# Kernel optimization log

Hardware: AMD Instinct MI355X
Metric: run time of the kernel (lower is better)

## Reference

```python
import jax, jax.numpy as jnp
import numpy as np

N_NODES = 150000
N_EDGES = 2400000
IN_DIM, HID, OUT_DIM = 2, 32, 1


def gcn_conv(x, edge_index, W, b, n_nodes):
    """PyG-style GCNConv: add self-loops, sym-normalize, aggregate, linear."""
    h = x @ W  # [N, F_out] linear first (as in PyG GCNConv)
    loop = jnp.arange(n_nodes)
    src = jnp.concatenate([edge_index[0], loop])
    dst = jnp.concatenate([edge_index[1], loop])
    deg = jax.ops.segment_sum(jnp.ones(src.shape[0], h.dtype), dst,
                              num_segments=n_nodes)  # in-degree incl. self-loops
    dinv = jnp.where(deg > 0, jax.lax.rsqrt(deg), 0.0)
    norm = dinv[src] * dinv[dst]  # [E+N]
    msg = h[src] * norm[:, None]  # gather + scale
    out = jax.ops.segment_sum(msg, dst, num_segments=n_nodes)  # scatter-add
    return out + b


def setup_inputs() -> dict:
    key = jax.random.key(0)
    ks = jax.random.split(key, 8)
    x = jax.random.normal(ks[0], (N_NODES, IN_DIM), dtype=jnp.float32)
    edge_index = jax.random.randint(ks[1], (2, N_EDGES), 0, N_NODES, dtype=jnp.int32)
    W1 = jax.random.normal(ks[2], (IN_DIM, HID), dtype=jnp.float32) / np.sqrt(IN_DIM)
    b1 = jnp.zeros((HID,), jnp.float32)
    W2 = jax.random.normal(ks[3], (HID, HID), dtype=jnp.float32) / np.sqrt(HID)
    b2 = jnp.zeros((HID,), jnp.float32)
    Wp = jax.random.normal(ks[4], (HID, OUT_DIM), dtype=jnp.float32) / np.sqrt(HID)
    bp = jnp.zeros((OUT_DIM,), jnp.float32)
    return {"x": x, "edge_index": edge_index, "W1": W1, "b1": b1,
            "W2": W2, "b2": b2, "Wp": Wp, "bp": bp}


def reference(x, edge_index, W1, b1, W2, b2, Wp, bp):
    n = x.shape[0]
    h = jax.nn.relu(gcn_conv(x, edge_index, W1, b1, n))
    h = jax.nn.relu(gcn_conv(h, edge_index, W2, b2, n))
    return jax.nn.sigmoid(h @ Wp + bp)  # [N, 1]
```

## Files before the change

### kernel.cpp

```cpp
#include <hip/hip_runtime.h>

#define HID 32
#define SH 9
#define BNODES 512
#define NBMAX 320
#define TILE 8192
#define CAP 16384
#define STAGECAP 12288

typedef unsigned int uint;

__device__ __forceinline__ uint f2bf(float v) {
    uint b = __float_as_uint(v);
    return (b + 0x7fffu + ((b >> 16) & 1u)) >> 16;
}

__global__ void k_zero(int* __restrict__ p, int n) {
    int i = blockIdx.x * 256 + threadIdx.x;
    if (i < n) p[i] = 0;
}

__global__ void __launch_bounds__(512) k_bucketize(
        const int* __restrict__ src, const int* __restrict__ dst,
        int* __restrict__ bcur, uint* __restrict__ ebuf, int E, int NB) {
    __shared__ uint  ecache[TILE];
    __shared__ unsigned short bcache[TILE];
    __shared__ int cnt[NBMAX];
    __shared__ int loff[NBMAX + 1];
    __shared__ int gbase[NBMAX];
    int tid = threadIdx.x;
    int tbase = blockIdx.x * TILE;
    int tcount = min(E - tbase, TILE);
    int tc4 = tcount >> 2;
    const int4* dst4 = (const int4*)(dst + tbase);
    const int4* src4 = (const int4*)(src + tbase);

    for (int b = tid; b < NBMAX; b += 512) cnt[b] = 0;
    __syncthreads();
#pragma unroll
    for (int k = 0; k < TILE / 4 / 512; ++k) {
        int q = k * 512 + tid;
        if (q < tc4) {
            int4 d = dst4[q];
            atomicAdd(&cnt[d.x >> SH], 1);
            atomicAdd(&cnt[d.y >> SH], 1);
            atomicAdd(&cnt[d.z >> SH], 1);
            atomicAdd(&cnt[d.w >> SH], 1);
        }
    }
    if (tid == 0)
        for (int t = tc4 << 2; t < tcount; ++t) atomicAdd(&cnt[dst[tbase + t] >> SH], 1);
    __syncthreads();
    if (tid < 64) {
        int lo = tid * 5;
        int s = 0;
        for (int b = lo; b < lo + 5 && b < NB; ++b) s += cnt[b];
        int v = s;
        for (int off = 1; off < 64; off <<= 1) {
            int u = __shfl_up(v, off, 64);
            if (tid >= off) v += u;
        }
        int excl = v - s;
        for (int b = lo; b < lo + 5 && b < NB; ++b) { loff[b] = excl; excl += cnt[b]; }
        if (tid == 63) loff[NB] = excl;
    }
    __syncthreads();
    for (int b = tid; b < NB; b += 512) cnt[b] = loff[b];
    __syncthreads();
#pragma unroll
    for (int k = 0; k < TILE / 4 / 512; ++k) {
        int q = k * 512 + tid;
        if (q < tc4) {
            int4 d = dst4[q];
            int4 s = src4[q];
            int b0 = d.x >> SH, p0 = atomicAdd(&cnt[b0], 1);
            ecache[p0] = (uint)s.x | ((uint)(d.x & (BNODES - 1)) << 18); bcache[p0] = (unsigned short)b0;
            int b1 = d.y >> SH, p1_ = atomicAdd(&cnt[b1], 1);
            ecache[p1_] = (uint)s.y | ((uint)(d.y & (BNODES - 1)) << 18); bcache[p1_] = (unsigned short)b1;
            int b2 = d.z >> SH, p2_ = atomicAdd(&cnt[b2], 1);
            ecache[p2_] = (uint)s.z | ((uint)(d.z & (BNODES - 1)) << 18); bcache[p2_] = (unsigned short)b2;
            int b3 = d.w >> SH, p3_ = atomicAdd(&cnt[b3], 1);
            ecache[p3_] = (uint)s.w | ((uint)(d.w & (BNODES - 1)) << 18); bcache[p3_] = (unsigned short)b3;
        }
    }
    if (tid == 0)
        for (int t = tc4 << 2; t < tcount; ++t) {
            int d = dst[tbase + t];
            int b_ = d >> SH;
            int pos = atomicAdd(&cnt[b_], 1);
            ecache[pos] = (uint)src[tbase + t] | ((uint)(d & (BNODES - 1)) << 18);
            bcache[pos] = (unsigned short)b_;
        }
    __syncthreads();
    for (int b = tid; b < NB; b += 512) {
        int tc = loff[b + 1] - loff[b];
        if (tc > 0) gbase[b] = b * CAP + atomicAdd(&bcur[b], tc);
    }
    __syncthreads();
    for (int j = tid; j < tcount; j += 512) {
        int b = bcache[j];
        ebuf[gbase[b] + (j - loff[b])] = ecache[j];
    }
}

__global__ void k_scanb(const int* __restrict__ bcur, int* __restrict__ bbase,
                        int* __restrict__ rowptr, int N, int NB) {
    __shared__ int l[NBMAX + 1];
    int tid = threadIdx.x;
    if (tid < 64) {
        int lo = tid * 5;
        int s = 0;
        for (int b = lo; b < lo + 5 && b < NB; ++b) s += bcur[b];
        int v = s;
        for (int off = 1; off < 64; off <<= 1) {
            int u = __shfl_up(v, off, 64);
            if (tid >= off) v += u;
        }
        int excl = v - s;
        for (int b = lo; b < lo + 5 && b < NB; ++b) { l[b] = excl; excl += bcur[b]; }
        if (tid == 63) l[NB] = excl;
    }
    __syncthreads();
    for (int b = tid; b <= NB; b += blockDim.x) bbase[b] = l[b];
    if (tid == 0) rowptr[N] = l[NB];
}

__global__ void __launch_bounds__(512) k_sortb(
        const uint* __restrict__ ebuf, const int* __restrict__ bcur,
        const int* __restrict__ bbase, const float* __restrict__ x,
        int* __restrict__ rowptr, float* __restrict__ dinv,
        float2* __restrict__ p1, int* __restrict__ col, int N) {
    __shared__ int c[BNODES];
    __shared__ int off[BNODES];
    __shared__ int cur[BNODES];
    __shared__ uint stage[STAGECAP];
    int b = blockIdx.x, tid = threadIdx.x;
    int cnt = bcur[b];
    const uint* eb = ebuf + (long)b * CAP;
    int cbase = bbase[b];
    for (int t = tid; t < BNODES; t += 512) c[t] = 0;
    __syncthreads();
    int vc = cnt >> 2;
    const uint4* e4 = (const uint4*)eb;
    for (int q = tid; q < vc; q += 512) {
        uint4 e = e4[q];
        atomicAdd(&c[e.x >> 18], 1);
        atomicAdd(&c[e.y >> 18], 1);
        atomicAdd(&c[e.z >> 18], 1);
        atomicAdd(&c[e.w >> 18], 1);
        int j = q << 2;
        if (j + 3 < STAGECAP) {
            stage[j] = e.x; stage[j + 1] = e.y; stage[j + 2] = e.z; stage[j + 3] = e.w;
        }
    }
    for (int j = (vc << 2) + tid; j < cnt; j += 512) {
        uint e = eb[j];
        atomicAdd(&c[e >> 18], 1);
        if (j < STAGECAP) stage[j] = e;
    }
    __syncthreads();
    if (tid < 64) {
        int lo = tid * 8, s = 0;
#pragma unroll
        for (int k = 0; k < 8; ++k) s += c[lo + k];
        int v = s;
        for (int o = 1; o < 64; o <<= 1) {
            int u = __shfl_up(v, o, 64);
            if (tid >= o) v += u;
        }
        int excl = v - s;
#pragma unroll
        for (int k = 0; k < 8; ++k) { off[lo + k] = excl; excl += c[lo + k]; }
    }
    __syncthreads();
    for (int t = tid; t < BNODES; t += 512) {
        cur[t] = off[t];
        int node = (b << SH) + t;
        if (node < N) {
            rowptr[node] = cbase + off[t];
            float di = rsqrtf((float)c[t] + 1.0f);
            dinv[node] = di;
            float2 xv = ((const float2*)x)[node];
            p1[node] = make_float2(xv.x * di, xv.y * di);
        }
    }
    __syncthreads();
    int lim = min(cnt, STAGECAP);
    for (int j = tid; j < lim; j += 512) {
        uint e = stage[j];
        int dl = e >> 18;
        int pos = atomicAdd(&cur[dl], 1);
        col[cbase + pos] = (int)(e & 0x3FFFF);
    }
    for (int j = STAGECAP + tid; j < cnt; j += 512) {
        uint e = eb[j];
        int dl = e >> 18;
        int pos = atomicAdd(&cur[dl], 1);
        col[cbase + pos] = (int)(e & 0x3FFFF);
    }
}

__global__ void __launch_bounds__(256) k_gl12(
        const int* __restrict__ rowptr, const int* __restrict__ col,
        const float2* __restrict__ p1, const float* __restrict__ dinv,
        const float* __restrict__ W1, const float* __restrict__ b1,
        const float* __restrict__ W2, uint* __restrict__ p2h, int N) {
    __shared__ float sW1[64], sb1[32], sW2[HID * HID];
    int tid = threadIdx.x;
    for (int t = tid; t < HID * HID; t += 256) sW2[t] = W2[t];
    if (tid < 64) sW1[tid] = W1[tid];
    if (tid < 32) sb1[tid] = b1[tid];
    __syncthreads();
    int i = blockIdx.x * 16 + (tid >> 4);
    if (i >= N) return;
    int sub = tid & 15;

    int beg = rowptr[i], end = rowptr[i + 1];
    float ax = 0, ay = 0, bx = 0, by = 0;
    int j = beg + sub;
    for (; j + 16 < end; j += 32) {
        int c0 = col[j], c1 = col[j + 16];
        float2 v0 = p1[c0], v1 = p1[c1];
        ax += v0.x; ay += v0.y;
        bx += v1.x; by += v1.y;
    }
    if (j < end) {
        float2 v = p1[col[j]];
        ax += v.x; ay += v.y;
    }
    float sx = ax + bx, sy = ay + by;
#pragma unroll
    for (int m = 1; m < 16; m <<= 1) {
        sx += __shfl_xor(sx, m, 16);
        sy += __shfl_xor(sy, m, 16);
    }

    float2 a = p1[i];
    float di = dinv[i];
    float g0 = di * (a.x + sx);
    float g1 = di * (a.y + sy);

    float h0 = fmaxf(g0 * sW1[2 * sub] + g1 * sW1[32 + 2 * sub] + sb1[2 * sub], 0.0f);
    float h1 = fmaxf(g0 * sW1[2 * sub + 1] + g1 * sW1[32 + 2 * sub + 1] + sb1[2 * sub + 1], 0.0f);

    float o0 = 0, o1 = 0;
    int fb = 2 * sub;
#pragma unroll
    for (int s = 0; s < 16; ++s) {
        float hk0 = __shfl(h0, s, 16);
        float hk1 = __shfl(h1, s, 16);
        const float* w0 = &sW2[(2 * s) * HID + fb];
        const float* w1 = &sW2[(2 * s + 1) * HID + fb];
        o0 += hk0 * w0[0]; o1 += hk0 * w0[1];
        o0 += hk1 * w1[0]; o1 += hk1 * w1[1];
    }

    p2h[(long)i * 16 + sub] = f2bf(di * o0) | (f2bf(di * o1) << 16);
}

__global__ void k_gout(const int* __restrict__ rowptr, const int* __restrict__ col,
                       const uint* __restrict__ p2h, const float* __restrict__ b2,
                       const float* __restrict__ Wp, const float* __restrict__ bp,
                       const float* __restrict__ dinv, float* __restrict__ out, int N) {
    int node = blockIdx.x * 16 + (threadIdx.x >> 4);
    if (node >= N) return;
    int hl = threadIdx.x & 15;
    int beg = rowptr[node], end = rowptr[node + 1];
    uint w = p2h[(long)node * 16 + hl];
    float sA0 = __uint_as_float(w << 16), sB0 = __uint_as_float(w & 0xffff0000u);
    float sA1 = 0, sB1 = 0, sA2 = 0, sB2 = 0, sA3 = 0, sB3 = 0;
    float sA4 = 0, sB4 = 0, sA5 = 0, sB5 = 0, sA6 = 0, sB6 = 0, sA7 = 0, sB7 = 0;
    int j = beg;
    for (; j + 8 <= end; j += 8) {
        int c0 = col[j],     c1 = col[j + 1], c2 = col[j + 2], c3 = col[j + 3];
        int c4 = col[j + 4], c5 = col[j + 5], c6 = col[j + 6], c7 = col[j + 7];
        uint w0 = p2h[(long)c0 * 16 + hl];
        uint w1 = p2h[(long)c1 * 16 + hl];
        uint w2 = p2h[(long)c2 * 16 + hl];
        uint w3 = p2h[(long)c3 * 16 + hl];
        uint w4 = p2h[(long)c4 * 16 + hl];
        uint w5 = p2h[(long)c5 * 16 + hl];
        uint w6 = p2h[(long)c6 * 16 + hl];
        uint w7 = p2h[(long)c7 * 16 + hl];
        sA0 += __uint_as_float(w0 << 16); sB0 += __uint_as_float(w0 & 0xffff0000u);
        sA1 += __uint_as_float(w1 << 16); sB1 += __uint_as_float(w1 & 0xffff0000u);
        sA2 += __uint_as_float(w2 << 16); sB2 += __uint_as_float(w2 & 0xffff0000u);
        sA3 += __uint_as_float(w3 << 16); sB3 += __uint_as_float(w3 & 0xffff0000u);
        sA4 += __uint_as_float(w4 << 16); sB4 += __uint_as_float(w4 & 0xffff0000u);
        sA5 += __uint_as_float(w5 << 16); sB5 += __uint_as_float(w5 & 0xffff0000u);
        sA6 += __uint_as_float(w6 << 16); sB6 += __uint_as_float(w6 & 0xffff0000u);
        sA7 += __uint_as_float(w7 << 16); sB7 += __uint_as_float(w7 & 0xffff0000u);
    }
    for (; j + 4 <= end; j += 4) {
        int c0 = col[j], c1 = col[j + 1], c2 = col[j + 2], c3 = col[j + 3];
        uint w0 = p2h[(long)c0 * 16 + hl];
        uint w1 = p2h[(long)c1 * 16 + hl];
        uint w2 = p2h[(long)c2 * 16 + hl];
        uint w3 = p2h[(long)c3 * 16 + hl];
        sA0 += __uint_as_float(w0 << 16); sB0 += __uint_as_float(w0 & 0xffff0000u);
        sA1 += __uint_as_float(w1 << 16); sB1 += __uint_as_float(w1 & 0xffff0000u);
        sA2 += __uint_as_float(w2 << 16); sB2 += __uint_as_float(w2 & 0xffff0000u);
        sA3 += __uint_as_float(w3 << 16); sB3 += __uint_as_float(w3 & 0xffff0000u);
    }
    for (; j < end; ++j) {
        uint wj = p2h[(long)col[j] * 16 + hl];
        sA0 += __uint_as_float(wj << 16); sB0 += __uint_as_float(wj & 0xffff0000u);
    }
    float sA = ((sA0 + sA1) + (sA2 + sA3)) + ((sA4 + sA5) + (sA6 + sA7));
    float sB = ((sB0 + sB1) + (sB2 + sB3)) + ((sB4 + sB5) + (sB6 + sB7));
    float di = dinv[node];
    float hvA = fmaxf(di * sA + b2[2 * hl], 0.0f);
    float hvB = fmaxf(di * sB + b2[2 * hl + 1], 0.0f);
    float v = hvA * Wp[2 * hl] + hvB * Wp[2 * hl + 1];
#pragma unroll
    for (int m = 8; m > 0; m >>= 1) v += __shfl_xor(v, m, 16);
    if (hl == 0) out[node] = 1.0f / (1.0f + expf(-(v + bp[0])));
}

extern "C" void kernel_launch(void* const* d_in, const int* in_sizes, int n_in,
                              void* d_out, int out_size, void* d_ws, size_t ws_size,
                              hipStream_t stream) {
    const float* x  = (const float*)d_in[0];
    const int*   ei = (const int*)d_in[1];
    const float* W1 = (const float*)d_in[2];
    const float* b1 = (const float*)d_in[3];
    const float* W2 = (const float*)d_in[4];
    const float* b2 = (const float*)d_in[5];
    const float* Wp = (const float*)d_in[6];
    const float* bp = (const float*)d_in[7];
    float* out = (float*)d_out;

    const int N = in_sizes[0] / 2;
    const int E = in_sizes[1] / 2;
    const int* src = ei;
    const int* dst = ei + E;
    const int NB = (N + BNODES - 1) >> SH;

    char* ws = (char*)d_ws;
    size_t off = 0;
    auto alloc = [&](size_t bytes) {
        void* ptr = ws + off;
        off += (bytes + 255) & ~(size_t)255;
        return ptr;
    };
    int*    bcur   = (int*)alloc((size_t)NBMAX * 4);
    int*    bbase  = (int*)alloc((size_t)(NBMAX + 1) * 4);
    int*    rowptr = (int*)alloc((size_t)(N + 1) * 4);
    float*  dinv   = (float*)alloc((size_t)N * 4);
    uint*   ebuf   = (uint*)alloc((size_t)NBMAX * CAP * 4);
    int*    col    = (int*)alloc((size_t)E * 4);
    float2* p1     = (float2*)alloc((size_t)N * 8);
    uint*   p2h    = (uint*)alloc((size_t)N * 16 * 4);

    const int nb_t = (E + TILE - 1) / TILE;
    const int nb_g = (N + 15) / 16;

    k_zero<<<(NBMAX + 255) / 256, 256, 0, stream>>>(bcur, NBMAX);
    k_bucketize<<<nb_t, 512, 0, stream>>>(src, dst, bcur, ebuf, E, NB);
    k_scanb<<<1, 256, 0, stream>>>(bcur, bbase, rowptr, N, NB);
    k_sortb<<<NB, 512, 0, stream>>>(ebuf, bcur, bbase, x, rowptr, dinv, p1, col, N);
    k_gl12<<<nb_g, 256, 0, stream>>>(rowptr, col, p1, dinv, W1, b1, W2, p2h, N);
    k_gout<<<nb_g, 256, 0, stream>>>(rowptr, col, p2h, b2, Wp, bp, dinv, out, N);
}
```

Measured before the change: 117.8 us.

## Sort nodes by degree within each bucket to balance aggregation work

In the bucket sort kernel, nodes in each 512-node bucket are counting-sorted by in-degree (capped at 63) into a node permutation. Both aggregation kernels then process nodes in that order, so the 16 nodes in a block and the 4 nodes in a wavefront have similar edge counts and less lane divergence and tail imbalance. The cost is an extra shared-memory histogram and scan in the sort kernel and one more indirection load per node group. Memory locality for rowptr and the output writes also becomes less regular.

```diff
diff --git a/kernel.cpp b/kernel.cpp
--- a/kernel.cpp
+++ b/kernel.cpp
@@ -129,16 +129,21 @@
         const uint* __restrict__ ebuf, const int* __restrict__ bcur,
         const int* __restrict__ bbase, const float* __restrict__ x,
         int* __restrict__ rowptr, float* __restrict__ dinv,
-        float2* __restrict__ p1, int* __restrict__ col, int N) {
+        float2* __restrict__ p1, int* __restrict__ col,
+        int* __restrict__ nodeperm, int N) {
     __shared__ int c[BNODES];
     __shared__ int off[BNODES];
     __shared__ int cur[BNODES];
+    __shared__ int dbin[64];
+    __shared__ int dcur[64];
     __shared__ uint stage[STAGECAP];
     int b = blockIdx.x, tid = threadIdx.x;
     int cnt = bcur[b];
     const uint* eb = ebuf + (long)b * CAP;
     int cbase = bbase[b];
+    int nnodes = min(BNODES, N - (b << SH));
     for (int t = tid; t < BNODES; t += 512) c[t] = 0;
+    if (tid < 64) dbin[tid] = 0;
     __syncthreads();
     int vc = cnt >> 2;
     const uint4* e4 = (const uint4*)eb;
@@ -183,6 +188,26 @@
             float2 xv = ((const float2*)x)[node];
             p1[node] = make_float2(xv.x * di, xv.y * di);
         }
+        if (t < nnodes) atomicAdd(&dbin[min(c[t], 63)], 1);
+    }
+    __syncthreads();
+    if (tid < 64) {
+        int orig = dbin[tid];
+        int v = orig;
+        for (int o = 1; o < 64; o <<= 1) {
+            int u = __shfl_up(v, o, 64);
+            if (tid >= o) v += u;
+        }
+        dcur[tid] = v - orig;
+    }
+    __syncthreads();
+    for (int t = tid; t < BNODES; t += 512) {
+        if (t < nnodes) {
+            int r = atomicAdd(&dcur[min(c[t], 63)], 1);
+            nodeperm[(b << SH) + r] = (b << SH) + t;
+        } else {
+            nodeperm[(b << SH) + t] = N;
+        }
     }
     __syncthreads();
     int lim = min(cnt, STAGECAP);
@@ -201,17 +226,20 @@
 }
 
 __global__ void __launch_bounds__(256) k_gl12(
+        const int* __restrict__ nodeperm,
         const int* __restrict__ rowptr, const int* __restrict__ col,
         const float2* __restrict__ p1, const float* __restrict__ dinv,
         const float* __restrict__ W1, const float* __restrict__ b1,
-        const float* __restrict__ W2, uint* __restrict__ p2h, int N) {
+        const float* __restrict__ W2, uint* __restrict__ p2h, int N, int NTOT) {
     __shared__ float sW1[64], sb1[32], sW2[HID * HID];
     int tid = threadIdx.x;
     for (int t = tid; t < HID * HID; t += 256) sW2[t] = W2[t];
     if (tid < 64) sW1[tid] = W1[tid];
     if (tid < 32) sb1[tid] = b1[tid];
     __syncthreads();
-    int i = blockIdx.x * 16 + (tid >> 4);
+    int idx = blockIdx.x * 16 + (tid >> 4);
+    if (idx >= NTOT) return;
+    int i = nodeperm[idx];
     if (i >= N) return;
     int sub = tid & 15;
 
@@ -258,11 +286,15 @@
     p2h[(long)i * 16 + sub] = f2bf(di * o0) | (f2bf(di * o1) << 16);
 }
 
-__global__ void k_gout(const int* __restrict__ rowptr, const int* __restrict__ col,
+__global__ void k_gout(const int* __restrict__ nodeperm,
+                       const int* __restrict__ rowptr, const int* __restrict__ col,
                        const uint* __restrict__ p2h, const float* __restrict__ b2,
                        const float* __restrict__ Wp, const float* __restrict__ bp,
-                       const float* __restrict__ dinv, float* __restrict__ out, int N) {
-    int node = blockIdx.x * 16 + (threadIdx.x >> 4);
+                       const float* __restrict__ dinv, float* __restrict__ out,
+                       int N, int NTOT) {
+    int idx = blockIdx.x * 16 + (threadIdx.x >> 4);
+    if (idx >= NTOT) return;
+    int node = nodeperm[idx];
     if (node >= N) return;
     int hl = threadIdx.x & 15;
     int beg = rowptr[node], end = rowptr[node + 1];
@@ -335,6 +367,7 @@
     const int* src = ei;
     const int* dst = ei + E;
     const int NB = (N + BNODES - 1) >> SH;
+    const int NTOT = NB << SH;
 
     char* ws = (char*)d_ws;
     size_t off = 0;
@@ -343,22 +376,23 @@
         off += (bytes + 255) & ~(size_t)255;
         return ptr;
     };
-    int*    bcur   = (int*)alloc((size_t)NBMAX * 4);
-    int*    bbase  = (int*)alloc((size_t)(NBMAX + 1) * 4);
-    int*    rowptr = (int*)alloc((size_t)(N + 1) * 4);
-    float*  dinv   = (float*)alloc((size_t)N * 4);
-    uint*   ebuf   = (uint*)alloc((size_t)NBMAX * CAP * 4);
-    int*    col    = (int*)alloc((size_t)E * 4);
-    float2* p1     = (float2*)alloc((size_t)N * 8);
-    uint*   p2h    = (uint*)alloc((size_t)N * 16 * 4);
+    int*    bcur     = (int*)alloc((size_t)NBMAX * 4);
+    int*    bbase    = (int*)alloc((size_t)(NBMAX + 1) * 4);
+    int*    rowptr   = (int*)alloc((size_t)(N + 1) * 4);
+    float*  dinv     = (float*)alloc((size_t)N * 4);
+    uint*   ebuf     = (uint*)alloc((size_t)NBMAX * CAP * 4);
+    int*    col      = (int*)alloc((size_t)E * 4);
+    float2* p1       = (float2*)alloc((size_t)N * 8);
+    uint*   p2h      = (uint*)alloc((size_t)N * 16 * 4);
+    int*    nodeperm = (int*)alloc((size_t)(NB << SH) * 4);
 
     const int nb_t = (E + TILE - 1) / TILE;
-    const int nb_g = (N + 15) / 16;
+    const int nb_p = (NTOT + 15) / 16;
 
     k_zero<<<(NBMAX + 255) / 256, 256, 0, stream>>>(bcur, NBMAX);
     k_bucketize<<<nb_t, 512, 0, stream>>>(src, dst, bcur, ebuf, E, NB);
     k_scanb<<<1, 256, 0, stream>>>(bcur, bbase, rowptr, N, NB);
-    k_sortb<<<NB, 512, 0, stream>>>(ebuf, bcur, bbase, x, rowptr, dinv, p1, col, N);
-    k_gl12<<<nb_g, 256, 0, stream>>>(rowptr, col, p1, dinv, W1, b1, W2, p2h, N);
-    k_gout<<<nb_g, 256, 0, stream>>>(rowptr, col, p2h, b2, Wp, bp, dinv, out, N);
-}
+    k_sortb<<<NB, 512, 0, stream>>>(ebuf, bcur, bbase, x, rowptr, dinv, p1, col, nodeperm, N);
+    k_gl12<<<nb_p, 256, 0, stream>>>(nodeperm, rowptr, col, p1, dinv, W1, b1, W2, p2h, N, NTOT);
+    k_gout<<<nb_p, 256, 0, stream>>>(nodeperm, rowptr, col, p2h, b2, Wp, bp, dinv, out, N, NTOT);
+}
```

Result: slower. 129.5 us (+9.9%).
